# Optimization experiments

Hardware: AMD Instinct MI355X
Metric: run time of the kernel (lower is better)

Reference implementation:

```python
import jax, jax.numpy as jnp
import numpy as np

HID, H, DK, DV, KS = 2048, 16, 128, 128, 4

def _p(key, shape, scale=0.02):
    return (jax.random.normal(key, shape, dtype=jnp.float32) * scale)

def setup_inputs() -> dict:
    key = jax.random.key(0)
    ks = jax.random.split(key, 20)
    B, T = 2, 2048
    x = jax.random.normal(ks[0], (B, T, HID), dtype=jnp.float32)
    inp = {
        'x': x,
        'Wq': _p(ks[1], (HID, H * DK)),
        'Wk': _p(ks[2], (HID, H * DK)),
        'Wv': _p(ks[3], (HID, H * DV)),
        'Wa': _p(ks[4], (HID, H)), 'ba': jnp.zeros((H,), jnp.float32),
        'Wb': _p(ks[5], (HID, H)), 'bb': jnp.zeros((H,), jnp.float32),
        'Wg': _p(ks[6], (HID, H * DV)),
        'Wo': _p(ks[7], (H * DV, HID)),
        'conv_q_w': _p(ks[8], (H * DK, 1, KS), 0.3), 'conv_q_b': jnp.zeros((H * DK,), jnp.float32),
        'conv_k_w': _p(ks[9], (H * DK, 1, KS), 0.3), 'conv_k_b': jnp.zeros((H * DK,), jnp.float32),
        'conv_v_w': _p(ks[10], (H * DV, 1, KS), 0.3), 'conv_v_b': jnp.zeros((H * DV,), jnp.float32),
        'ln_w': jnp.ones((DV,), jnp.float32), 'ln_b': jnp.zeros((DV,), jnp.float32),
    }
    return inp

def _dwconv_causal(y, w, b):
    # y: [B,T,C]; depthwise causal conv (torch pads K-1 both sides then slices [:T])
    out = jax.lax.conv_general_dilated(
        y.transpose(0, 2, 1), w, window_strides=(1,),
        padding=[(KS - 1, 0)], feature_group_count=w.shape[0])
    return out.transpose(0, 2, 1) + b

def _silu(x):
    return x * jax.nn.sigmoid(x)

def _gated_delta(q, k, v, alpha, beta, scale):
    # q,k,v: [B,T,H,D]; alpha,beta: [B,T,H]
    B, T, nH, _ = q.shape
    qs = q.transpose(1, 0, 2, 3)  # [T,B,H,Dk]
    ks = k.transpose(1, 0, 2, 3) * scale
    vs = v.transpose(1, 0, 2, 3)
    al = alpha.transpose(1, 0, 2)  # [T,B,H]
    be = beta.transpose(1, 0, 2)

    def step(S, inp):
        qt, kt, vt, at, bt = inp
        err = jnp.einsum('bhvk,bhk->bhv', S, kt) - vt
        S = at[..., None, None] * S - bt[..., None, None] * err[..., None] * kt[:, :, None, :]
        o = jnp.einsum('bhvk,bhk->bhv', S, qt)
        return S, o

    S0 = jnp.zeros((B, nH, DV, DK), dtype=q.dtype)
    _, o = jax.lax.scan(step, S0, (qs, ks, vs, al, be))
    return o.transpose(1, 0, 2, 3)  # [B,T,H,Dv]

def reference(x, Wq, Wk, Wv, Wa, ba, Wb, bb, Wg, Wo,
              conv_q_w, conv_q_b, conv_k_w, conv_k_b, conv_v_w, conv_v_b,
              ln_w, ln_b):
    B, T, _ = x.shape
    scale = DK ** -0.5
    q = _silu(_dwconv_causal(x @ Wq, conv_q_w, conv_q_b))
    k = _silu(_dwconv_causal(x @ Wk, conv_k_w, conv_k_b))
    v = _silu(_dwconv_causal(x @ Wv, conv_v_w, conv_v_b))
    q = q.reshape(B, T, H, DK)
    k = k.reshape(B, T, H, DK)
    v = v.reshape(B, T, H, DV)
    alpha = jax.nn.sigmoid(x @ Wa + ba)
    beta = jax.nn.sigmoid(x @ Wb + bb)
    o = _gated_delta(q, k, v, alpha, beta, scale)  # [B,T,H,Dv]
    # LayerNorm over last dim (eps=1e-5)
    mu = o.mean(-1, keepdims=True)
    var = ((o - mu) ** 2).mean(-1, keepdims=True)
    o = (o - mu) * jax.lax.rsqrt(var + 1e-5) * ln_w + ln_b
    g = jax.nn.sigmoid(x @ Wg).reshape(B, T, H, DV)
    o = (o * g).reshape(B, T, H * DV)
    return o @ Wo
```

## Files before the change

kernel.cpp:

```cpp
#include <hip/hip_runtime.h>
#include <hip/hip_bf16.h>


#define HIDN 2048
#define NH   16
#define BB   2
#define TT   2048
#define MR   (BB*TT)
#define NPROJ 8192
#define REC  400
#define CHUNK 16

typedef __attribute__((ext_vector_type(8))) short short8;
typedef __attribute__((ext_vector_type(4))) float f32x4;

__device__ __forceinline__ unsigned short f2bf(float f) {
  union { float f; unsigned u; } x; x.f = f;
  unsigned r = x.u + 0x7fffu + ((x.u >> 16) & 1u);
  return (unsigned short)(r >> 16);
}
__device__ __forceinline__ float bf2f(unsigned short u) {
  union { unsigned u; float f; } x; x.u = ((unsigned)u) << 16;
  return x.f;
}

__device__ __forceinline__ void gload16(const void* g, void* l) {
  __builtin_amdgcn_global_load_lds(
      (const __attribute__((address_space(1))) unsigned int*)g,
      (__attribute__((address_space(3))) unsigned int*)l, 16, 0, 0);
}

__device__ __forceinline__ float sigmoidf_(float v) { return 1.f / (1.f + __expf(-v)); }

template<int CTRL>
__device__ __forceinline__ float dppadd(float x) {
  union { float f; int i; } a, b;
  a.f = x;
  b.i = __builtin_amdgcn_update_dpp(0, a.i, CTRL, 0xf, 0xf, true);
  return a.f + b.f;
}
__device__ __forceinline__ float red16(float x) {
  x = dppadd<0x128>(x);
  x = dppadd<0x124>(x);
  x = dppadd<0x122>(x);
  x = dppadd<0x121>(x);
  return x;
}

__global__ __launch_bounds__(256) void cvt_f32_bf16(const float* __restrict__ in,
                                                    unsigned short* __restrict__ out) {
  int i = blockIdx.x * 256 + threadIdx.x;
  float4 v = ((const float4*)in)[i];
  ushort4 u;
  u.x = f2bf(v.x); u.y = f2bf(v.y); u.z = f2bf(v.z); u.w = f2bf(v.w);
  ((ushort4*)out)[i] = u;
}

struct TPtrs { const float* src[5]; unsigned short* dst[5]; };

__global__ __launch_bounds__(256) void transpose_cvt(TPtrs p) {
  __shared__ float tile[32][33];
  const float* src = p.src[blockIdx.z];
  unsigned short* dst = p.dst[blockIdx.z];
  int c0 = blockIdx.x * 32, r0 = blockIdx.y * 32;
  int lx = threadIdx.x & 31, ly = threadIdx.x >> 5;
#pragma unroll
  for (int i = 0; i < 32; i += 8)
    tile[ly + i][lx] = src[(size_t)(r0 + ly + i) * 2048 + c0 + lx];
  __syncthreads();
#pragma unroll
  for (int i = 0; i < 32; i += 8)
    dst[(size_t)(c0 + ly + i) * 2048 + r0 + lx] = f2bf(tile[lx][ly + i]);
}

template<int OUT_BF16>
__global__ __launch_bounds__(256) void gemm_bt(const unsigned short* __restrict__ A,
                                               const unsigned short* __restrict__ BT,
                                               void* __restrict__ C, int K, int ldc) {
  __shared__ unsigned short lA[128 * 64];
  __shared__ unsigned short lB[128 * 64];
  const int tid = threadIdx.x;
  const int wave = tid >> 6, lane = tid & 63;
  const int m0 = blockIdx.x * 128, n0 = blockIdx.y * 128;
  const int wm = wave >> 1, wn = wave & 1;
  const int lr = lane & 15, lk = (lane >> 4) * 8;
  const int srow = (lane >> 3), scol = (lane & 7) * 8;
  f32x4 acc[4][4] = {};
  for (int k0 = 0; k0 < K; k0 += 64) {
    __syncthreads();
#pragma unroll
    for (int c = 0; c < 4; ++c) {
      int seg = wave * 4 + c;
      int row = seg * 8 + srow;
      gload16(A + (size_t)(m0 + row) * K + k0 + scol, (void*)(lA + seg * 512));
      gload16(BT + (size_t)(n0 + row) * K + k0 + scol, (void*)(lB + seg * 512));
    }
    asm volatile("s_waitcnt vmcnt(0)" ::: "memory");
    __syncthreads();
#pragma unroll
    for (int kk = 0; kk < 2; ++kk) {
      short8 af[4], bg[4];
#pragma unroll
      for (int mi = 0; mi < 4; ++mi)
        af[mi] = *(const short8*)&lA[(wm * 64 + mi * 16 + lr) * 64 + kk * 32 + lk];
#pragma unroll
      for (int ni = 0; ni < 4; ++ni)
        bg[ni] = *(const short8*)&lB[(wn * 64 + ni * 16 + lr) * 64 + kk * 32 + lk];
#pragma unroll
      for (int mi = 0; mi < 4; ++mi)
#pragma unroll
        for (int ni = 0; ni < 4; ++ni)
          acc[mi][ni] = __builtin_amdgcn_mfma_f32_16x16x32_bf16(af[mi], bg[ni], acc[mi][ni], 0, 0, 0);
    }
  }
  const int orow = (lane >> 4) * 4, ocol = lane & 15;
#pragma unroll
  for (int mi = 0; mi < 4; ++mi)
#pragma unroll
    for (int ni = 0; ni < 4; ++ni) {
      int rbase = m0 + wm * 64 + mi * 16 + orow;
      int cc = n0 + wn * 64 + ni * 16 + ocol;
#pragma unroll
      for (int j = 0; j < 4; ++j) {
        if (OUT_BF16)
          ((unsigned short*)C)[(size_t)(rbase + j) * ldc + cc] = f2bf(acc[mi][ni][j]);
        else
          ((float*)C)[(size_t)(rbase + j) * ldc + cc] = acc[mi][ni][j];
      }
    }
}

__global__ __launch_bounds__(256) void gemv_ab(const float* __restrict__ x,
                                               const float* __restrict__ Wa, const float* __restrict__ ba,
                                               const float* __restrict__ Wb, const float* __restrict__ bb,
                                               float* __restrict__ qkvab) {
  __shared__ float red[2][4][16][16];
  int tid = threadIdx.x;
  int h = tid & 15, grp = tid >> 4;
  int m0 = blockIdx.x * 4;
  float aa[4] = {0, 0, 0, 0}, bbv[4] = {0, 0, 0, 0};
  for (int kk = 0; kk < 128; ++kk) {
    int k = grp + kk * 16;
    float wa = Wa[k * 16 + h], wb = Wb[k * 16 + h];
#pragma unroll
    for (int r = 0; r < 4; ++r) {
      float xv = x[(size_t)(m0 + r) * HIDN + k];
      aa[r] += xv * wa; bbv[r] += xv * wb;
    }
  }
#pragma unroll
  for (int r = 0; r < 4; ++r) { red[0][r][grp][h] = aa[r]; red[1][r][grp][h] = bbv[r]; }
  __syncthreads();
  if (tid < 128) {
    int hh = tid & 15, ab = (tid >> 4) & 1, r = tid >> 5;
    float s = 0.f;
#pragma unroll
    for (int g = 0; g < 16; ++g) s += red[ab][r][g][hh];
    s += ab ? bb[hh] : ba[hh];
    s = sigmoidf_(s);
    int m = m0 + r; int b = m >> 11, t = m & 2047;
    qkvab[((size_t)(b * NH + hh) * TT + t) * REC + 384 + ab] = s;
  }
}

struct ConvPtrs { const float* w[3]; const float* bias[3]; };

__global__ __launch_bounds__(256) void conv_silu(const unsigned short* __restrict__ Y, ConvPtrs p,
                                                 float kscale, float* __restrict__ qkvab) {
  int proj = blockIdx.y;
  int idx = blockIdx.x * 256 + threadIdx.x;
  int c = idx & 2047;
  int t = (idx >> 11) & 2047;
  int b = idx >> 22;
  const float* w = p.w[proj] + c * 4;
  float acc = p.bias[proj][c];
  const unsigned short* ycol = Y + (size_t)(b * TT) * NPROJ + proj * 2048 + c;
#pragma unroll
  for (int i = 0; i < 4; ++i) {
    int tt = t - 3 + i;
    if (tt >= 0) acc += w[i] * bf2f(ycol[(size_t)tt * NPROJ]);
  }
  float s = acc * sigmoidf_(acc);
  if (proj == 1) s *= kscale;
  int hh = c >> 7, d = c & 127;
  qkvab[((size_t)(b * NH + hh) * TT + t) * REC + proj * 128 + d] = s;
}

__global__ __launch_bounds__(256, 1) void scan_kernel(const float* __restrict__ qkvab,
                                                      unsigned short* __restrict__ o) {
  __shared__ float buf[2][CHUNK * REC];
  int bh = blockIdx.x & 31;
  int vg = blockIdx.x >> 5;
  int tid = threadIdx.x;
  int wave = tid >> 6, lane = tid & 63;
  int r = tid >> 4, s = tid & 15;
  const float* stream = qkvab + (size_t)bh * TT * REC;
  int b = bh >> 4, h = bh & 15;
  unsigned short* op = o + ((size_t)b * TT * NH + h) * 128 + vg * 16 + r;
  float S[8] = {0, 0, 0, 0, 0, 0, 0, 0};
  float pob[CHUNK];
  for (int c = wave; c < 25; c += 4)
    gload16(stream + c * 256 + lane * 4, (void*)(&buf[0][0] + c * 256));
  asm volatile("s_waitcnt vmcnt(0)" ::: "memory");
  __syncthreads();
  for (int ch = 0; ch < TT / CHUNK; ++ch) {
    int pb = ch & 1;
    if (ch + 1 < TT / CHUNK) {
      const float* src = stream + (size_t)(ch + 1) * CHUNK * REC;
      for (int c = wave; c < 25; c += 4)
        gload16(src + c * 256 + lane * 4, (void*)(&buf[pb ^ 1][0] + c * 256));
    }
    if (ch > 0 && s == 0) {
      int tb = (ch - 1) * CHUNK;
#pragma unroll
      for (int j = 0; j < CHUNK; ++j)
        op[(size_t)(tb + j) * (NH * 128)] = f2bf(pob[j]);
    }
    const float* rec = &buf[pb][0];
#pragma unroll
    for (int st = 0; st < CHUNK; ++st) {
      const float* rr = rec + st * REC;
      float4 k0 = *(const float4*)&rr[128 + s * 4];
      float4 k1 = *(const float4*)&rr[192 + s * 4];
      float4 q0 = *(const float4*)&rr[s * 4];
      float4 q1 = *(const float4*)&rr[64 + s * 4];
      float vt = rr[256 + vg * 16 + r];
      float al = rr[384], be = rr[385];
      float a0 = S[0] * k0.x, a1 = S[1] * k0.y, a2 = S[2] * k0.z, a3 = S[3] * k0.w;
      float a4 = S[4] * k1.x, a5 = S[5] * k1.y, a6 = S[6] * k1.z, a7 = S[7] * k1.w;
      float p = ((a0 + a1) + (a2 + a3)) + ((a4 + a5) + (a6 + a7));
      p = red16(p);
      float c2 = be * (p - vt);
      S[0] = al * S[0] - c2 * k0.x;
      S[1] = al * S[1] - c2 * k0.y;
      S[2] = al * S[2] - c2 * k0.z;
      S[3] = al * S[3] - c2 * k0.w;
      S[4] = al * S[4] - c2 * k1.x;
      S[5] = al * S[5] - c2 * k1.y;
      S[6] = al * S[6] - c2 * k1.z;
      S[7] = al * S[7] - c2 * k1.w;
      float b0 = S[0] * q0.x, b1 = S[1] * q0.y, b2 = S[2] * q0.z, b3 = S[3] * q0.w;
      float b4 = S[4] * q1.x, b5 = S[5] * q1.y, b6 = S[6] * q1.z, b7 = S[7] * q1.w;
      float po = ((b0 + b1) + (b2 + b3)) + ((b4 + b5) + (b6 + b7));
      po = red16(po);
      pob[st] = po;
    }
    asm volatile("s_waitcnt vmcnt(0)" ::: "memory");
    __syncthreads();
  }
  if (s == 0) {
    int tb = (TT / CHUNK - 1) * CHUNK;
#pragma unroll
    for (int j = 0; j < CHUNK; ++j)
      op[(size_t)(tb + j) * (NH * 128)] = f2bf(pob[j]);
  }
}

__global__ __launch_bounds__(64) void ln_gate(const unsigned short* __restrict__ o,
                                              const unsigned short* __restrict__ Y,
                                              const float* __restrict__ lnw, const float* __restrict__ lnb,
                                              unsigned short* __restrict__ og) {
  int idx = blockIdx.x;
  int h = idx & 15; int bt = idx >> 4;
  int lane = threadIdx.x;
  const unsigned short* ob = o + (size_t)idx * 128;
  float o0 = bf2f(ob[lane]), o1 = bf2f(ob[lane + 64]);
  float s = o0 + o1, s2 = o0 * o0 + o1 * o1;
#pragma unroll
  for (int m = 1; m < 64; m <<= 1) { s += __shfl_xor(s, m); s2 += __shfl_xor(s2, m); }
  float mu = s * (1.f / 128.f);
  float var = s2 * (1.f / 128.f) - mu * mu;
  float rstd = rsqrtf(var + 1e-5f);
  const unsigned short* yg = Y + (size_t)bt * NPROJ + 6144 + h * 128;
  float g0 = sigmoidf_(bf2f(yg[lane])), g1 = sigmoidf_(bf2f(yg[lane + 64]));
  float r0 = ((o0 - mu) * rstd * lnw[lane] + lnb[lane]) * g0;
  float r1 = ((o1 - mu) * rstd * lnw[lane + 64] + lnb[lane + 64]) * g1;
  unsigned short* ogb = og + (size_t)bt * HIDN + h * 128;
  ogb[lane] = f2bf(r0); ogb[lane + 64] = f2bf(r1);
}

extern "C" void kernel_launch(void* const* d_in, const int* in_sizes, int n_in,
                              void* d_out, int out_size, void* d_ws, size_t ws_size,
                              hipStream_t stream) {
  (void)in_sizes; (void)n_in; (void)out_size;
  const float* x   = (const float*)d_in[0];
  const float* Wq  = (const float*)d_in[1];
  const float* Wk  = (const float*)d_in[2];
  const float* Wv  = (const float*)d_in[3];
  const float* Wa  = (const float*)d_in[4];
  const float* ba  = (const float*)d_in[5];
  const float* Wb  = (const float*)d_in[6];
  const float* bb  = (const float*)d_in[7];
  const float* Wg  = (const float*)d_in[8];
  const float* Wo  = (const float*)d_in[9];
  const float* cqw = (const float*)d_in[10];
  const float* cqb = (const float*)d_in[11];
  const float* ckw = (const float*)d_in[12];
  const float* ckb = (const float*)d_in[13];
  const float* cvw = (const float*)d_in[14];
  const float* cvb = (const float*)d_in[15];
  const float* lnw = (const float*)d_in[16];
  const float* lnb = (const float*)d_in[17];

  size_t need = 0;
  size_t o_WT    = need; need += (size_t)NPROJ * HIDN * 2;
  size_t o_WoT   = need; need += (size_t)HIDN * HIDN * 2;
  size_t o_Y     = need; need += (size_t)MR * NPROJ * 2;
  size_t o_qkvab = need; need += (size_t)BB * NH * TT * REC * 4;
  size_t o_xog   = need; need += (size_t)MR * HIDN * 2;
  size_t o_obf   = need; need += (size_t)MR * HIDN * 2;
  if (need > ws_size) return;

  char* ws = (char*)d_ws;
  unsigned short* WT_all = (unsigned short*)(ws + o_WT);
  unsigned short* WoT    = (unsigned short*)(ws + o_WoT);
  unsigned short* Y_all  = (unsigned short*)(ws + o_Y);
  float*          qkvab  = (float*)(ws + o_qkvab);
  unsigned short* x_bf   = (unsigned short*)(ws + o_xog);
  unsigned short* og     = (unsigned short*)(ws + o_xog);
  unsigned short* o_bf   = (unsigned short*)(ws + o_obf);

  cvt_f32_bf16<<<(MR * HIDN) / 4 / 256, 256, 0, stream>>>(x, x_bf);

  TPtrs tp;
  tp.src[0] = Wq; tp.src[1] = Wk; tp.src[2] = Wv; tp.src[3] = Wg; tp.src[4] = Wo;
  tp.dst[0] = WT_all;
  tp.dst[1] = WT_all + (size_t)2048 * 2048;
  tp.dst[2] = WT_all + (size_t)2 * 2048 * 2048;
  tp.dst[3] = WT_all + (size_t)3 * 2048 * 2048;
  tp.dst[4] = WoT;
  transpose_cvt<<<dim3(64, 64, 5), 256, 0, stream>>>(tp);

  gemv_ab<<<MR / 4, 256, 0, stream>>>(x, Wa, ba, Wb, bb, qkvab);

  gemm_bt<1><<<dim3(MR / 128, NPROJ / 128), 256, 0, stream>>>(x_bf, WT_all, (void*)Y_all, HIDN, NPROJ);

  ConvPtrs cp;
  cp.w[0] = cqw; cp.w[1] = ckw; cp.w[2] = cvw;
  cp.bias[0] = cqb; cp.bias[1] = ckb; cp.bias[2] = cvb;
  conv_silu<<<dim3((BB * TT * 2048) / 256, 3), 256, 0, stream>>>(Y_all, cp, 0.08838834764831845f, qkvab);

  scan_kernel<<<256, 256, 0, stream>>>(qkvab, o_bf);

  ln_gate<<<MR * NH, 64, 0, stream>>>(o_bf, Y_all, lnw, lnb, og);

  gemm_bt<0><<<dim3(MR / 128, HIDN / 128), 256, 0, stream>>>(og, WoT, d_out, HIDN, HIDN);
}
```

Baseline: 1.010 ms.

## Split scan state across 32 lanes per row and double the block count

Each scan block now covers 8 value rows instead of 16, and each row is spread over 32 lanes holding 4 state elements apiece instead of 16 lanes holding 8. The grid doubles to 512 blocks and launch bounds allow two blocks per CU, so more of the device works on the serial recurrence and each step has a shorter dependency chain. The k·S reduction becomes a 32-lane reduce (DPP plus a ds_swizzle). The q·S half-reduction is deferred: it is completed with a swizzle only when the chunk's outputs are written. The cost is that every block re-streams the same q/k/v/alpha/beta records, so global and LDS traffic for those records doubles, and the extra cross-row swizzle adds latency to each step.

```diff
diff --git a/kernel.cpp b/kernel.cpp
--- a/kernel.cpp
+++ b/kernel.cpp
@@ -45,6 +45,16 @@
   x = dppadd<0x122>(x);
   x = dppadd<0x121>(x);
   return x;
+}
+__device__ __forceinline__ float swz16(float x) {
+  union { float f; int i; } a, b;
+  a.f = x;
+  b.i = __builtin_amdgcn_ds_swizzle(a.i, 0x401f);
+  return b.f;
+}
+__device__ __forceinline__ float red32(float x) {
+  x = red16(x);
+  return x + swz16(x);
 }
 
 __global__ __launch_bounds__(256) void cvt_f32_bf16(const float* __restrict__ in,
@@ -186,18 +196,18 @@
   qkvab[((size_t)(b * NH + hh) * TT + t) * REC + proj * 128 + d] = s;
 }
 
-__global__ __launch_bounds__(256, 1) void scan_kernel(const float* __restrict__ qkvab,
+__global__ __launch_bounds__(256, 2) void scan_kernel(const float* __restrict__ qkvab,
                                                       unsigned short* __restrict__ o) {
   __shared__ float buf[2][CHUNK * REC];
   int bh = blockIdx.x & 31;
   int vg = blockIdx.x >> 5;
   int tid = threadIdx.x;
   int wave = tid >> 6, lane = tid & 63;
-  int r = tid >> 4, s = tid & 15;
+  int r = tid >> 5, s = tid & 31;
   const float* stream = qkvab + (size_t)bh * TT * REC;
   int b = bh >> 4, h = bh & 15;
-  unsigned short* op = o + ((size_t)b * TT * NH + h) * 128 + vg * 16 + r;
-  float S[8] = {0, 0, 0, 0, 0, 0, 0, 0};
+  unsigned short* op = o + ((size_t)b * TT * NH + h) * 128 + vg * 8 + r;
+  float S0 = 0.f, S1 = 0.f, S2 = 0.f, S3 = 0.f;
   float pob[CHUNK];
   for (int c = wave; c < 25; c += 4)
     gload16(stream + c * 256 + lane * 4, (void*)(&buf[0][0] + c * 256));
@@ -210,49 +220,42 @@
       for (int c = wave; c < 25; c += 4)
         gload16(src + c * 256 + lane * 4, (void*)(&buf[pb ^ 1][0] + c * 256));
     }
-    if (ch > 0 && s == 0) {
+    if (ch > 0) {
       int tb = (ch - 1) * CHUNK;
 #pragma unroll
-      for (int j = 0; j < CHUNK; ++j)
-        op[(size_t)(tb + j) * (NH * 128)] = f2bf(pob[j]);
+      for (int j = 0; j < CHUNK; ++j) {
+        float full = pob[j] + swz16(pob[j]);
+        if (s == 0) op[(size_t)(tb + j) * (NH * 128)] = f2bf(full);
+      }
     }
     const float* rec = &buf[pb][0];
 #pragma unroll
     for (int st = 0; st < CHUNK; ++st) {
       const float* rr = rec + st * REC;
-      float4 k0 = *(const float4*)&rr[128 + s * 4];
-      float4 k1 = *(const float4*)&rr[192 + s * 4];
-      float4 q0 = *(const float4*)&rr[s * 4];
-      float4 q1 = *(const float4*)&rr[64 + s * 4];
-      float vt = rr[256 + vg * 16 + r];
+      float4 kk = *(const float4*)&rr[128 + s * 4];
+      float4 qq = *(const float4*)&rr[s * 4];
+      float vt = rr[256 + vg * 8 + r];
       float al = rr[384], be = rr[385];
-      float a0 = S[0] * k0.x, a1 = S[1] * k0.y, a2 = S[2] * k0.z, a3 = S[3] * k0.w;
-      float a4 = S[4] * k1.x, a5 = S[5] * k1.y, a6 = S[6] * k1.z, a7 = S[7] * k1.w;
-      float p = ((a0 + a1) + (a2 + a3)) + ((a4 + a5) + (a6 + a7));
-      p = red16(p);
+      float p = (S0 * kk.x + S1 * kk.y) + (S2 * kk.z + S3 * kk.w);
+      p = red32(p);
       float c2 = be * (p - vt);
-      S[0] = al * S[0] - c2 * k0.x;
-      S[1] = al * S[1] - c2 * k0.y;
-      S[2] = al * S[2] - c2 * k0.z;
-      S[3] = al * S[3] - c2 * k0.w;
-      S[4] = al * S[4] - c2 * k1.x;
-      S[5] = al * S[5] - c2 * k1.y;
-      S[6] = al * S[6] - c2 * k1.z;
-      S[7] = al * S[7] - c2 * k1.w;
-      float b0 = S[0] * q0.x, b1 = S[1] * q0.y, b2 = S[2] * q0.z, b3 = S[3] * q0.w;
-      float b4 = S[4] * q1.x, b5 = S[5] * q1.y, b6 = S[6] * q1.z, b7 = S[7] * q1.w;
-      float po = ((b0 + b1) + (b2 + b3)) + ((b4 + b5) + (b6 + b7));
-      po = red16(po);
-      pob[st] = po;
+      S0 = al * S0 - c2 * kk.x;
+      S1 = al * S1 - c2 * kk.y;
+      S2 = al * S2 - c2 * kk.z;
+      S3 = al * S3 - c2 * kk.w;
+      float po = (S0 * qq.x + S1 * qq.y) + (S2 * qq.z + S3 * qq.w);
+      pob[st] = red16(po);
     }
     asm volatile("s_waitcnt vmcnt(0)" ::: "memory");
     __syncthreads();
   }
-  if (s == 0) {
+  {
     int tb = (TT / CHUNK - 1) * CHUNK;
 #pragma unroll
-    for (int j = 0; j < CHUNK; ++j)
-      op[(size_t)(tb + j) * (NH * 128)] = f2bf(pob[j]);
+    for (int j = 0; j < CHUNK; ++j) {
+      float full = pob[j] + swz16(pob[j]);
+      if (s == 0) op[(size_t)(tb + j) * (NH * 128)] = f2bf(full);
+    }
   }
 }
 
@@ -340,7 +343,7 @@
   cp.bias[0] = cqb; cp.bias[1] = ckb; cp.bias[2] = cvb;
   conv_silu<<<dim3((BB * TT * 2048) / 256, 3), 256, 0, stream>>>(Y_all, cp, 0.08838834764831845f, qkvab);
 
-  scan_kernel<<<256, 256, 0, stream>>>(qkvab, o_bf);
+  scan_kernel<<<512, 256, 0, stream>>>(qkvab, o_bf);
 
   ln_gate<<<MR * NH, 64, 0, stream>>>(o_bf, Y_all, lnw, lnb, og);
 
```

Measured after the change: 1.101 ms. +9.1%, slower.
